# Performance work log

Measured on AMD Instinct MI355X. Metric: run time of the kernel, lower is better.

Reference implementation:

```python
import jax, jax.numpy as jnp
import numpy as np

N_ATOMS = 10000
N_EDGES = 200000
L_MAX = 2
K_L = [32, 24, 16]  # k_max_l = n_element_channels * n_max_l

# (l1, l2, L) in the original loop order (l1 outer, l2 inner, L ascending)
PAIRS = [(0,0,0),(0,1,1),(0,2,2),
         (1,0,1),(1,1,0),(1,1,1),(1,1,2),(1,2,1),(1,2,2),
         (2,0,2),(2,1,1),(2,1,2),(2,2,0),(2,2,1),(2,2,2)]
# concatenated input width -> k_max_l[L] per (L, sigma) channel
LIN = {'0_1': (72, 32), '1_1': (80, 24), '1_m1': (40, 24), '2_1': (72, 16), '2_m1': (32, 16)}


def setup_inputs() -> dict:
    key = jax.random.key(0)
    it = iter(jax.random.split(key, 64))
    def nrm(shape):
        return jax.random.normal(next(it), shape, dtype=jnp.float32)
    inp = {}
    for l in range(L_MAX + 1):
        inp['rb%d' % l] = nrm((N_EDGES, K_L[l]))           # radial basis per l
    for l in range(L_MAX + 1):
        inp['sh%d' % l] = nrm((N_EDGES, 2*l+1, 1))         # spherical harmonics per l
    inp['emb'] = nrm((N_ATOMS, 1, K_L[0]))                 # initial center embedding
    for l in range(L_MAX + 1):
        inp['f%d' % l] = nrm((N_ATOMS, 2*l+1, K_L[l]))     # nu=1 equivariant features
    for (l1, l2, L) in PAIRS:
        inp['cg_%d_%d_%d' % (l1, l2, L)] = nrm(((2*l1+1)*(2*l2+1), 2*L+1))
    for LS, (fin, fout) in LIN.items():
        inp['W_' + LS] = nrm((fin, fout)) / np.float32(np.sqrt(fin))
        inp['b_' + LS] = nrm((fout,)) * 0.01
    inp['centers'] = jax.random.randint(next(it), (N_EDGES,), 0, N_ATOMS)
    inp['neighbors'] = jax.random.randint(next(it), (N_EDGES,), 0, N_ATOMS)
    inp['n_atoms'] = N_ATOMS
    return inp


def _normalize(x, dims):
    # Normalizer(dims): RMS normalization over the given dims
    return x * jax.lax.rsqrt(jnp.mean(x * x, axis=dims, keepdims=True) + 1e-12)


def _forward(floats, centers, neighbors, n_atoms):
    (rb0, rb1, rb2, sh0, sh1, sh2, emb, f0, f1, f2,
     cg_0_0_0, cg_0_1_1, cg_0_2_2, cg_1_0_1, cg_1_1_0, cg_1_1_1, cg_1_1_2,
     cg_1_2_1, cg_1_2_2, cg_2_0_2, cg_2_1_1, cg_2_1_2, cg_2_2_0, cg_2_2_1,
     cg_2_2_2, W_0_1, b_0_1, W_1_1, b_1_1, W_1_m1, b_1_m1, W_2_1, b_2_1,
     W_2_m1, b_2_m1) = floats
    rb = [rb0, rb1, rb2]; sh = [sh0, sh1, sh2]; feats = [f0, f1, f2]
    cgs = {'0_0_0': cg_0_0_0, '0_1_1': cg_0_1_1, '0_2_2': cg_0_2_2,
           '1_0_1': cg_1_0_1, '1_1_0': cg_1_1_0, '1_1_1': cg_1_1_1,
           '1_1_2': cg_1_1_2, '1_2_1': cg_1_2_1, '1_2_2': cg_1_2_2,
           '2_0_2': cg_2_0_2, '2_1_1': cg_2_1_1, '2_1_2': cg_2_1_2,
           '2_2_0': cg_2_2_0, '2_2_1': cg_2_2_1, '2_2_2': cg_2_2_2}
    lin = {'0_1': (W_0_1, b_0_1), '1_1': (W_1_1, b_1_1), '1_m1': (W_1_m1, b_1_m1),
           '2_1': (W_2_1, b_2_1), '2_m1': (W_2_m1, b_2_m1)}

    # ---- InvariantMessagePasser: density_l = scatter_add over centers of
    #      sh_l * rb_l * emb[neighbors]
    emb_n = emb[neighbors]                                       # [E, 1, k0]
    densities = []
    for l in range(L_MAX + 1):
        msg = sh[l] * rb[l][:, None, :] * emb_n[:, :, :K_L[l]]   # [E, 2l+1, k_l]
        densities.append(jax.ops.segment_sum(msg, centers, num_segments=n_atoms))

    # ---- EquivariantMessagePasser
    ve = [sh[l] * rb[l][:, None, :] for l in range(L_MAX + 1)]   # vector expansion [E,2l+1,k_l]
    fn = [feats[l][neighbors] for l in range(L_MAX + 1)]         # gathered neighbor feats
    results = {}
    for (l1, l2, L) in PAIRS:
        S = (-1) ** (l1 + l2 + L)
        k = min(K_L[l1], K_L[l2])
        t1 = ve[l1][:, :, :k]                                    # [E, 2l1+1, k]
        t2 = fn[l2][:, :, :k]                                    # [E, 2l2+1, k]
        cg = cgs['%d_%d_%d' % (l1, l2, L)].reshape(2*l1+1, 2*l2+1, 2*L+1)
        # fused outer product + CG contraction -> [E, 2L+1, k]
        res = jnp.einsum('eak,ebk,abM->eMk', t1, t2, cg)
        pooled = jax.ops.segment_sum(res, centers, num_segments=n_atoms)
        LS = '%d_%s' % (L, 'm1' if S < 0 else '1')
        results.setdefault(LS, []).append(pooled)

    outs = {}
    for LS, (W, b) in lin.items():
        x = jnp.concatenate(results[LS], axis=2)                 # [n_atoms, 2L+1, size_LS]
        x = _normalize(x, (0, 1))
        x = jnp.einsum('amf,fk->amk', x, W) + b
        outs[LS] = _normalize(x, (0, 1, 2))

    return (densities[0], densities[1], densities[2],
            outs['0_1'], outs['1_1'], outs['1_m1'], outs['2_1'], outs['2_m1'])


def reference(rb0, rb1, rb2, sh0, sh1, sh2, emb, f0, f1, f2,
              cg_0_0_0, cg_0_1_1, cg_0_2_2, cg_1_0_1, cg_1_1_0, cg_1_1_1,
              cg_1_1_2, cg_1_2_1, cg_1_2_2, cg_2_0_2, cg_2_1_1, cg_2_1_2,
              cg_2_2_0, cg_2_2_1, cg_2_2_2, W_0_1, b_0_1, W_1_1, b_1_1,
              W_1_m1, b_1_m1, W_2_1, b_2_1, W_2_m1, b_2_m1,
              centers, neighbors, n_atoms):
    floats = (rb0, rb1, rb2, sh0, sh1, sh2, emb, f0, f1, f2,
              cg_0_0_0, cg_0_1_1, cg_0_2_2, cg_1_0_1, cg_1_1_0, cg_1_1_1,
              cg_1_1_2, cg_1_2_1, cg_1_2_2, cg_2_0_2, cg_2_1_1, cg_2_1_2,
              cg_2_2_0, cg_2_2_1, cg_2_2_2, W_0_1, b_0_1, W_1_1, b_1_1,
              W_1_m1, b_1_m1, W_2_1, b_2_1, W_2_m1, b_2_m1)
    return _forward(floats, centers, neighbors, n_atoms)
```

## Files before the change

kernel.cpp:

```cpp
#include <hip/hip_runtime.h>
#include <hip/hip_bf16.h>

typedef __hip_bfloat16 bf16;

#define N_ATOMS 10000
#define N_EDGES 200000

#define SCG   0
#define SINV  616
#define SS1P  1024
#define SS2P  19968
#define SWS2  20288
#define SINTS 20352
#define IFLAG  0
#define ICOUNT 16
#define IOFFS  10016
#define ICURS  20032
#define IELIST 30032
#define INTS_END 430032
#define SXACC (SINTS + INTS_END)
#define BIG_FLOATS (SXACC + 952*N_ATOMS)

#define O0 0
#define O1 320000
#define O2 1040000
#define OY 1840000
#define OUT_ELEMS 5200000

__device__ __forceinline__ float b2f(bf16 x){ return __bfloat162float(x); }
__device__ __forceinline__ bf16  f2b(float x){ return __float2bfloat16(x); }

__device__ __forceinline__ float ldv(const float* p, int i){ return p[i]; }
__device__ __forceinline__ float ldv(const bf16*  p, int i){ return b2f(p[i]); }
__device__ __forceinline__ void  stv(float* p, int i, float v){ p[i] = v; }
__device__ __forceinline__ void  stv(bf16*  p, int i, float v){ p[i] = f2b(v); }

template<typename T> __device__ __forceinline__ int dtid();
template<> __device__ __forceinline__ int dtid<bf16>(){ return 0; }
template<> __device__ __forceinline__ int dtid<float>(){ return 1; }

struct Ptrs15 { const void* p[15]; };
struct LinP   { const void* W[5]; const void* B[5]; };

__constant__ int c_cg_sizes[15] = {1,9,25,9,9,27,45,45,75,25,45,75,25,75,125};
__constant__ int c_fin[5]   = {72,80,40,72,32};
__constant__ int c_kout[5]  = {32,24,24,16,16};
__constant__ int c_yoff[5]  = {OY+0, OY+320000, OY+1040000, OY+1760000, OY+2560000};
__constant__ int c_numel[5] = {320000,720000,720000,800000,800000};
__constant__ int c_cum[6]   = {0,32,104,176,256,336};
__constant__ int c_xb[5]    = {0,72,312,432,792};
__constant__ int c_Ms[5]    = {1,3,3,5,5};

__global__ void k_zero(float* wsf, int* wsi,
                       const unsigned short* rb0u, const unsigned short* embu) {
  if (blockIdx.x == 0 && threadIdx.x < 64) {
    int lane = threadIdx.x;
    int bad = 0;
    for (int i = lane; i < 256; i += 64) {
      unsigned u1 = ((unsigned)rb0u[2*i]) << 16;
      unsigned u2 = ((unsigned)embu[2*i]) << 16;
      float v1 = __uint_as_float(u1);
      float v2 = __uint_as_float(u2);
      if (!(fabsf(v1) < 1e9f) || !(fabsf(v2) < 1e9f)) bad = 1;
    }
    unsigned long long any = __ballot(bad);
    if (lane == 0) wsi[IFLAG] = (any != 0ULL) ? 1 : 0;
  }
  int i = blockIdx.x*blockDim.x + threadIdx.x;
  if (i < N_ATOMS) wsi[ICOUNT + i] = 0;
  int j = i - N_ATOMS;
  if (j >= 0 && j < N_ATOMS) wsi[ICURS + j] = 0;
  j -= N_ATOMS;
  if (j >= 0 && j < 18944) wsf[SS1P + j] = 0.f;
  j -= 18944;
  if (j >= 0 && j < 325) wsf[SS2P + j] = 0.f;
}

template<typename T>
__global__ void k_cg(Ptrs15 cg, float* wsf, const int* flag) {
  if (flag[0] != dtid<T>()) return;
  int i = blockIdx.x*blockDim.x + threadIdx.x;
  if (i >= 615) return;
  int s = 0, off = i;
  while (off >= c_cg_sizes[s]) { off -= c_cg_sizes[s]; ++s; }
  wsf[SCG + i] = ldv((const T*)cg.p[s], off);
}

__global__ void k_hist(const int* __restrict__ centers, int* __restrict__ counts) {
  int e = blockIdx.x*blockDim.x + threadIdx.x;
  if (e < N_EDGES) atomicAdd(&counts[centers[e]], 1);
}

__global__ void k_scan(const int* __restrict__ counts, int* __restrict__ offs) {
  __shared__ int part[1024];
  int t = threadIdx.x;
  int base = t*10;
  int s = 0;
  for (int i = 0; i < 10; ++i) { int idx = base+i; if (idx < N_ATOMS) s += counts[idx]; }
  part[t] = s;
  __syncthreads();
  for (int d = 1; d < 1024; d <<= 1) {
    int v = part[t];
    int add = (t >= d) ? part[t-d] : 0;
    __syncthreads();
    part[t] = v + add;
    __syncthreads();
  }
  int run = (t == 0) ? 0 : part[t-1];
  for (int i = 0; i < 10; ++i) {
    int idx = base+i;
    if (idx < N_ATOMS) { offs[idx] = run; run += counts[idx]; }
  }
  if (t == 1023) offs[N_ATOMS] = part[1023];
}

__global__ void k_scatter2(const int* __restrict__ centers, const int* __restrict__ neighbors,
                           const int* __restrict__ offs, int* __restrict__ cursors,
                           int2* __restrict__ elist2) {
  int e = blockIdx.x*blockDim.x + threadIdx.x;
  if (e < N_EDGES) {
    int c = centers[e];
    int p = atomicAdd(&cursors[c], 1);
    elist2[offs[c] + p] = make_int2(e, neighbors[e]);
  }
}

template<typename T>
__device__ __forceinline__ void role_body(
    const T* __restrict__ rb0, const T* __restrict__ rb1, const T* __restrict__ rb2,
    const T* __restrict__ sh0, const T* __restrict__ sh1, const T* __restrict__ sh2,
    const T* __restrict__ emb, const T* __restrict__ f0, const T* __restrict__ f1,
    const T* __restrict__ f2, const int2* __restrict__ el2,
    const int* __restrict__ offs, Ptrs15 cg,
    float* __restrict__ s1p, float* __restrict__ xout, T* __restrict__ out)
{
  int lane = threadIdx.x & 63;
  int role = threadIdx.x >> 6;
  int bid = blockIdx.x;
  int a = (bid & 7) * 1250 + (bid >> 3);
  int beg = offs[a];
  int cnt = offs[a+1] - beg;
  const int2* eb = el2 + beg;
  int ab = a & 63;
  int k32 = lane & 31, e2 = lane >> 5;
  int k16 = lane & 15, e4 = lane >> 4;
  float* xg = xout + a*952;
  float* s1r = s1p + ab*296;

  if (role == 0) {
    float acc[8];
    #pragma unroll
    for (int i = 0; i < 8; ++i) acc[i] = 0.f;
    for (int base = 0; base < cnt; base += 4) {
      #pragma unroll
      for (int u = 0; u < 2; ++u) {
        int idx = base + 2*u + e2;
        float w = (idx < cnt) ? 1.f : 0.f;
        int ic  = (idx < cnt) ? idx : 0;
        int2 en = eb[ic];
        int e = en.x, n = en.y;
        float s0 = ldv(sh0, e);
        float s1a0 = ldv(sh1, e*3+0), s1a1 = ldv(sh1, e*3+1), s1a2 = ldv(sh1, e*3+2);
        float rb0k = ldv(rb0, e*32 + k32) * w;
        float ek   = ldv(emb, n*32 + k32);
        float f0k  = ldv(f0,  n*32 + k32);
        float ve0 = s0 * rb0k;
        acc[0] = fmaf(ve0, ek, acc[0]);
        acc[4] = fmaf(ve0, f0k, acc[4]);
        if (k32 < 24) {
          float rb1k = ldv(rb1, e*24 + k32) * w;
          float rbek = rb1k * ek;
          acc[1] = fmaf(s1a0, rbek, acc[1]);
          acc[2] = fmaf(s1a1, rbek, acc[2]);
          acc[3] = fmaf(s1a2, rbek, acc[3]);
          float f1k0 = ldv(f1, n*72 + k32);
          float f1k1 = ldv(f1, n*72 + 24 + k32);
          float f1k2 = ldv(f1, n*72 + 48 + k32);
          acc[5] = fmaf(ve0, f1k0, acc[5]);
          acc[6] = fmaf(ve0, f1k1, acc[6]);
          acc[7] = fmaf(ve0, f1k2, acc[7]);
        }
      }
    }
    #pragma unroll
    for (int i = 0; i < 8; ++i) acc[i] += __shfl_xor(acc[i], 32);
    const T* C000 = (const T*)cg.p[0];
    const T* C011 = (const T*)cg.p[1];
    float x000 = ldv(C000,0) * acc[4];
    float x011[3];
    #pragma unroll
    for (int M = 0; M < 3; ++M) {
      float t = 0.f;
      #pragma unroll
      for (int b = 0; b < 3; ++b) t = fmaf(acc[5+b], ldv(C011, b*3+M), t);
      x011[M] = t;
    }
    if (lane < 32) {
      stv(out, O0 + a*32 + k32, acc[0]);
      xg[k32] = x000;
      atomicAdd(&s1r[k32], x000*x000);
      if (k32 < 24) {
        #pragma unroll
        for (int m = 0; m < 3; ++m) stv(out, O1 + a*72 + m*24 + k32, acc[1+m]);
        #pragma unroll
        for (int M = 0; M < 3; ++M) xg[72+M*80+k32] = x011[M];
        atomicAdd(&s1r[72+k32], x011[0]*x011[0]+x011[1]*x011[1]+x011[2]*x011[2]);
      }
    }
  } else if (role == 1) {
    float acc[12];
    #pragma unroll
    for (int i = 0; i < 12; ++i) acc[i] = 0.f;
    int k24 = (k32 < 24) ? k32 : 23;
    float m24 = (k32 < 24) ? 1.f : 0.f;
    for (int base = 0; base < cnt; base += 4) {
      #pragma unroll
      for (int u = 0; u < 2; ++u) {
        int idx = base + 2*u + e2;
        float w = ((idx < cnt) ? 1.f : 0.f) * m24;
        int ic  = (idx < cnt) ? idx : 0;
        int2 en = eb[ic];
        int e = en.x, n = en.y;
        float s1a0 = ldv(sh1, e*3+0), s1a1 = ldv(sh1, e*3+1), s1a2 = ldv(sh1, e*3+2);
        float rb1k = ldv(rb1, e*24 + k24) * w;
        float f0k  = ldv(f0,  n*32 + k24);
        float f1k0 = ldv(f1, n*72 + k24);
        float f1k1 = ldv(f1, n*72 + 24 + k24);
        float f1k2 = ldv(f1, n*72 + 48 + k24);
        float g3 = rb1k * f0k;
        acc[0] = fmaf(g3, s1a0, acc[0]);
        acc[1] = fmaf(g3, s1a1, acc[1]);
        acc[2] = fmaf(g3, s1a2, acc[2]);
        float sa;
        sa = rb1k * s1a0;
        acc[3] = fmaf(sa, f1k0, acc[3]); acc[4] = fmaf(sa, f1k1, acc[4]); acc[5] = fmaf(sa, f1k2, acc[5]);
        sa = rb1k * s1a1;
        acc[6] = fmaf(sa, f1k0, acc[6]); acc[7] = fmaf(sa, f1k1, acc[7]); acc[8] = fmaf(sa, f1k2, acc[8]);
        sa = rb1k * s1a2;
        acc[9] = fmaf(sa, f1k0, acc[9]); acc[10] = fmaf(sa, f1k1, acc[10]); acc[11] = fmaf(sa, f1k2, acc[11]);
      }
    }
    #pragma unroll
    for (int i = 0; i < 12; ++i) acc[i] += __shfl_xor(acc[i], 32);
    const T* C101 = (const T*)cg.p[3];
    const T* C110 = (const T*)cg.p[4];
    const T* C111 = (const T*)cg.p[5];
    const T* C112 = (const T*)cg.p[6];
    float x101[3], x111[3], x112[5], x110;
    #pragma unroll
    for (int M = 0; M < 3; ++M) {
      float t = 0.f;
      #pragma unroll
      for (int aa = 0; aa < 3; ++aa) t = fmaf(acc[aa], ldv(C101, aa*3+M), t);
      x101[M] = t;
    }
    {
      float t = 0.f;
      #pragma unroll
      for (int q = 0; q < 9; ++q) t = fmaf(acc[3+q], ldv(C110, q), t);
      x110 = t;
    }
    #pragma unroll
    for (int M = 0; M < 3; ++M) {
      float t = 0.f;
      #pragma unroll
      for (int q = 0; q < 9; ++q) t = fmaf(acc[3+q], ldv(C111, q*3+M), t);
      x111[M] = t;
    }
    #pragma unroll
    for (int M = 0; M < 5; ++M) {
      float t = 0.f;
      #pragma unroll
      for (int q = 0; q < 9; ++q) t = fmaf(acc[3+q], ldv(C112, q*5+M), t);
      x112[M] = t;
    }
    if (lane < 24) {
      xg[32+k32] = x110;
      #pragma unroll
      for (int M = 0; M < 3; ++M) xg[72+M*80+24+k32] = x101[M];
      #pragma unroll
      for (int M = 0; M < 3; ++M) xg[312+M*40+k32]   = x111[M];
      #pragma unroll
      for (int M = 0; M < 5; ++M) xg[432+M*72+16+k32] = x112[M];
      atomicAdd(&s1r[32+k32], x110*x110);
      atomicAdd(&s1r[96+k32], x101[0]*x101[0]+x101[1]*x101[1]+x101[2]*x101[2]);
      atomicAdd(&s1r[152+k32], x111[0]*x111[0]+x111[1]*x111[1]+x111[2]*x111[2]);
      atomicAdd(&s1r[208+k32], x112[0]*x112[0]+x112[1]*x112[1]+x112[2]*x112[2]
                              + x112[3]*x112[3]+x112[4]*x112[4]);
    }
  } else if (role == 2) {
    float acc[25];
    #pragma unroll
    for (int i = 0; i < 25; ++i) acc[i] = 0.f;
    for (int base = 0; base < cnt; base += 8) {
      #pragma unroll
      for (int u = 0; u < 2; ++u) {
        int idx = base + 4*u + e4;
        float w = (idx < cnt) ? 1.f : 0.f;
        int ic  = (idx < cnt) ? idx : 0;
        int2 en = eb[ic];
        int e = en.x, n = en.y;
        float s0 = ldv(sh0, e);
        float s1a[3];
        #pragma unroll
        for (int m = 0; m < 3; ++m) s1a[m] = ldv(sh1, e*3+m);
        float s2a[5];
        #pragma unroll
        for (int m = 0; m < 5; ++m) s2a[m] = ldv(sh2, e*5+m);
        float rb0k = ldv(rb0, e*32 + k16) * w;
        float rb1k = ldv(rb1, e*24 + k16) * w;
        float rb2k = ldv(rb2, e*16 + k16) * w;
        float ek   = ldv(emb, n*32 + k16);
        float f2k[5];
        #pragma unroll
        for (int b = 0; b < 5; ++b) f2k[b] = ldv(f2, n*80 + b*16 + k16);
        float re = rb2k * ek;
        #pragma unroll
        for (int m = 0; m < 5; ++m) acc[m] = fmaf(s2a[m], re, acc[m]);
        float ve0 = s0 * rb0k;
        #pragma unroll
        for (int b = 0; b < 5; ++b) acc[5+b] = fmaf(ve0, f2k[b], acc[5+b]);
        #pragma unroll
        for (int aa = 0; aa < 3; ++aa) {
          float sa = rb1k * s1a[aa];
          #pragma unroll
          for (int b = 0; b < 5; ++b)
            acc[10+aa*5+b] = fmaf(sa, f2k[b], acc[10+aa*5+b]);
        }
      }
    }
    #pragma unroll
    for (int i = 0; i < 25; ++i) {
      acc[i] += __shfl_xor(acc[i], 16);
      acc[i] += __shfl_xor(acc[i], 32);
    }
    const T* C022 = (const T*)cg.p[2];
    const T* C121 = (const T*)cg.p[7];
    const T* C122 = (const T*)cg.p[8];
    float x022[5], x121[3], x122[5];
    #pragma unroll
    for (int M = 0; M < 5; ++M) {
      float t = 0.f;
      #pragma unroll
      for (int b = 0; b < 5; ++b) t = fmaf(acc[5+b], ldv(C022, b*5+M), t);
      x022[M] = t;
    }
    #pragma unroll
    for (int M = 0; M < 3; ++M) {
      float t = 0.f;
      #pragma unroll
      for (int q = 0; q < 15; ++q) t = fmaf(acc[10+q], ldv(C121, q*3+M), t);
      x121[M] = t;
    }
    #pragma unroll
    for (int M = 0; M < 5; ++M) {
      float t = 0.f;
      #pragma unroll
      for (int q = 0; q < 15; ++q) t = fmaf(acc[10+q], ldv(C122, q*5+M), t);
      x122[M] = t;
    }
    if (lane < 16) {
      #pragma unroll
      for (int m = 0; m < 5; ++m) stv(out, O2 + a*80 + m*16 + k16, acc[m]);
      #pragma unroll
      for (int M = 0; M < 5; ++M) xg[432+M*72+k16]   = x022[M];
      #pragma unroll
      for (int M = 0; M < 3; ++M) xg[72+M*80+48+k16] = x121[M];
      #pragma unroll
      for (int M = 0; M < 5; ++M) xg[792+M*32+k16]   = x122[M];
      atomicAdd(&s1r[192+k16], x022[0]*x022[0]+x022[1]*x022[1]+x022[2]*x022[2]
                              + x022[3]*x022[3]+x022[4]*x022[4]);
      atomicAdd(&s1r[120+k16], x121[0]*x121[0]+x121[1]*x121[1]+x121[2]*x121[2]);
      atomicAdd(&s1r[264+k16], x122[0]*x122[0]+x122[1]*x122[1]+x122[2]*x122[2]
                              + x122[3]*x122[3]+x122[4]*x122[4]);
    }
  } else if (role == 3) {
    float acc[20];
    #pragma unroll
    for (int i = 0; i < 20; ++i) acc[i] = 0.f;
    for (int base = 0; base < cnt; base += 8) {
      #pragma unroll
      for (int u = 0; u < 2; ++u) {
        int idx = base + 4*u + e4;
        float w = (idx < cnt) ? 1.f : 0.f;
        int ic  = (idx < cnt) ? idx : 0;
        int2 en = eb[ic];
        int e = en.x, n = en.y;
        float s2a[5];
        #pragma unroll
        for (int m = 0; m < 5; ++m) s2a[m] = ldv(sh2, e*5+m);
        float rb2k = ldv(rb2, e*16 + k16) * w;
        float f0k  = ldv(f0,  n*32 + k16);
        float f1k[3];
        #pragma unroll
        for (int b = 0; b < 3; ++b) f1k[b] = ldv(f1, n*72 + b*24 + k16);
        float g9 = rb2k * f0k;
        #pragma unroll
        for (int aa = 0; aa < 5; ++aa) acc[aa] = fmaf(g9, s2a[aa], acc[aa]);
        #pragma unroll
        for (int aa = 0; aa < 5; ++aa) {
          float sa = rb2k * s2a[aa];
          #pragma unroll
          for (int b = 0; b < 3; ++b)
            acc[5+aa*3+b] = fmaf(sa, f1k[b], acc[5+aa*3+b]);
        }
      }
    }
    #pragma unroll
    for (int i = 0; i < 20; ++i) {
      acc[i] += __shfl_xor(acc[i], 16);
      acc[i] += __shfl_xor(acc[i], 32);
    }
    const T* C202 = (const T*)cg.p[9];
    const T* C211 = (const T*)cg.p[10];
    const T* C212 = (const T*)cg.p[11];
    float x202[5], x211[3], x212[5];
    #pragma unroll
    for (int M = 0; M < 5; ++M) {
      float t = 0.f;
      #pragma unroll
      for (int aa = 0; aa < 5; ++aa) t = fmaf(acc[aa], ldv(C202, aa*5+M), t);
      x202[M] = t;
    }
    #pragma unroll
    for (int M = 0; M < 3; ++M) {
      float t = 0.f;
      #pragma unroll
      for (int q = 0; q < 15; ++q) t = fmaf(acc[5+q], ldv(C211, q*3+M), t);
      x211[M] = t;
    }
    #pragma unroll
    for (int M = 0; M < 5; ++M) {
      float t = 0.f;
      #pragma unroll
      for (int q = 0; q < 15; ++q) t = fmaf(acc[5+q], ldv(C212, q*5+M), t);
      x212[M] = t;
    }
    if (lane < 16) {
      #pragma unroll
      for (int M = 0; M < 5; ++M) xg[432+M*72+40+k16] = x202[M];
      #pragma unroll
      for (int M = 0; M < 3; ++M) xg[72+M*80+64+k16]  = x211[M];
      #pragma unroll
      for (int M = 0; M < 5; ++M) xg[792+M*32+16+k16] = x212[M];
      atomicAdd(&s1r[232+k16], x202[0]*x202[0]+x202[1]*x202[1]+x202[2]*x202[2]
                              + x202[3]*x202[3]+x202[4]*x202[4]);
      atomicAdd(&s1r[136+k16], x211[0]*x211[0]+x211[1]*x211[1]+x211[2]*x211[2]);
      atomicAdd(&s1r[280+k16], x212[0]*x212[0]+x212[1]*x212[1]+x212[2]*x212[2]
                              + x212[3]*x212[3]+x212[4]*x212[4]);
    }
  } else {
    float acc[25];
    #pragma unroll
    for (int i = 0; i < 25; ++i) acc[i] = 0.f;
    for (int base = 0; base < cnt; base += 8) {
      #pragma unroll
      for (int u = 0; u < 2; ++u) {
        int idx = base + 4*u + e4;
        float w = (idx < cnt) ? 1.f : 0.f;
        int ic  = (idx < cnt) ? idx : 0;
        int2 en = eb[ic];
        int e = en.x, n = en.y;
        float s2a[5];
        #pragma unroll
        for (int m = 0; m < 5; ++m) s2a[m] = ldv(sh2, e*5+m);
        float rb2k = ldv(rb2, e*16 + k16) * w;
        float f2k[5];
        #pragma unroll
        for (int b = 0; b < 5; ++b) f2k[b] = ldv(f2, n*80 + b*16 + k16);
        #pragma unroll
        for (int aa = 0; aa < 5; ++aa) {
          float sa = rb2k * s2a[aa];
          #pragma unroll
          for (int b = 0; b < 5; ++b)
            acc[aa*5+b] = fmaf(sa, f2k[b], acc[aa*5+b]);
        }
      }
    }
    #pragma unroll
    for (int i = 0; i < 25; ++i) {
      acc[i] += __shfl_xor(acc[i], 16);
      acc[i] += __shfl_xor(acc[i], 32);
    }
    const T* C220 = (const T*)cg.p[12];
    const T* C221 = (const T*)cg.p[13];
    const T* C222 = (const T*)cg.p[14];
    float x220, x221[3], x222[5];
    {
      float t = 0.f;
      #pragma unroll
      for (int q = 0; q < 25; ++q) t = fmaf(acc[q], ldv(C220, q), t);
      x220 = t;
    }
    #pragma unroll
    for (int M = 0; M < 3; ++M) {
      float t = 0.f;
      #pragma unroll
      for (int q = 0; q < 25; ++q) t = fmaf(acc[q], ldv(C221, q*3+M), t);
      x221[M] = t;
    }
    #pragma unroll
    for (int M = 0; M < 5; ++M) {
      float t = 0.f;
      #pragma unroll
      for (int q = 0; q < 25; ++q) t = fmaf(acc[q], ldv(C222, q*5+M), t);
      x222[M] = t;
    }
    if (lane < 16) {
      xg[56+k16] = x220;
      #pragma unroll
      for (int M = 0; M < 3; ++M) xg[312+M*40+24+k16] = x221[M];
      #pragma unroll
      for (int M = 0; M < 5; ++M) xg[432+M*72+56+k16] = x222[M];
      atomicAdd(&s1r[56+k16], x220*x220);
      atomicAdd(&s1r[176+k16], x221[0]*x221[0]+x221[1]*x221[1]+x221[2]*x221[2]);
      atomicAdd(&s1r[248+k16], x222[0]*x222[0]+x222[1]*x222[1]+x222[2]*x222[2]
                              + x222[3]*x222[3]+x222[4]*x222[4]);
    }
  }
}

__global__ __launch_bounds__(320) void k_role(
    const void* rb0, const void* rb1, const void* rb2,
    const void* sh0, const void* sh1, const void* sh2,
    const void* emb, const void* f0, const void* f1, const void* f2,
    const int2* __restrict__ el2, const int* __restrict__ offs, Ptrs15 cg,
    float* __restrict__ s1p, float* __restrict__ xout, void* outv,
    const int* __restrict__ flag, int know)
{
  int dt = (know >= 0) ? know : flag[0];
  if (dt == 0)
    role_body<bf16>((const bf16*)rb0,(const bf16*)rb1,(const bf16*)rb2,
                    (const bf16*)sh0,(const bf16*)sh1,(const bf16*)sh2,
                    (const bf16*)emb,(const bf16*)f0,(const bf16*)f1,(const bf16*)f2,
                    el2, offs, cg, s1p, xout, (bf16*)outv);
  else
    role_body<float>((const float*)rb0,(const float*)rb1,(const float*)rb2,
                     (const float*)sh0,(const float*)sh1,(const float*)sh2,
                     (const float*)emb,(const float*)f0,(const float*)f1,(const float*)f2,
                     el2, offs, cg, s1p, xout, (float*)outv);
}

template<typename T>
__device__ __forceinline__ void lin_body(
    const float* __restrict__ xg, const float* __restrict__ inv,
    LinP lp, T* __restrict__ out, float* __restrict__ s2p)
{
  int a = blockIdx.x;
  int t = threadIdx.x;
  __shared__ float L[952];
  for (int i = t; i < 952; i += 256) {
    int ch;
    if      (i < 72)  ch = i;
    else if (i < 312) ch = 72  + (i-72)  % 80;
    else if (i < 432) ch = 152 + (i-312) % 40;
    else if (i < 792) ch = 192 + (i-432) % 72;
    else              ch = 264 + (i-792) % 32;
    L[i] = xg[a*952 + i] * inv[ch];
  }
  __syncthreads();
  float y2[5] = {0.f,0.f,0.f,0.f,0.f};
  for (int tau = t; tau < 336; tau += 256) {
    int ls = 0;
    while (tau >= c_cum[ls+1]) ++ls;
    int rem = tau - c_cum[ls];
    int kn = c_kout[ls], fin = c_fin[ls];
    int M = rem / kn, ko = rem - M*kn;
    const T* W = (const T*)lp.W[ls];
    float y = ldv((const T*)lp.B[ls], ko);
    const float* xv = &L[c_xb[ls] + M*fin];
    for (int f = 0; f < fin; ++f) y = fmaf(xv[f], ldv(W, f*kn+ko), y);
    stv(out, c_yoff[ls] + (a*c_Ms[ls] + M)*kn + ko, y);
    y2[ls] += y*y;
  }
  __shared__ float red[4][5];
  #pragma unroll
  for (int i = 0; i < 5; ++i) {
    y2[i] += __shfl_xor(y2[i], 1);  y2[i] += __shfl_xor(y2[i], 2);
    y2[i] += __shfl_xor(y2[i], 4);  y2[i] += __shfl_xor(y2[i], 8);
    y2[i] += __shfl_xor(y2[i], 16); y2[i] += __shfl_xor(y2[i], 32);
  }
  if ((t & 63) == 0) {
    #pragma unroll
    for (int i = 0; i < 5; ++i) red[t>>6][i] = y2[i];
  }
  __syncthreads();
  if (t == 0) {
    #pragma unroll
    for (int i = 0; i < 5; ++i)
      atomicAdd(&s2p[i*64 + (a & 63)], red[0][i]+red[1][i]+red[2][i]+red[3][i]);
  }
}

__global__ __launch_bounds__(256) void k_lin(
    const float* __restrict__ xg, const float* __restrict__ inv,
    LinP lp, void* outv, float* __restrict__ s2p,
    const int* __restrict__ flag, int know)
{
  int dt = (know >= 0) ? know : flag[0];
  if (dt == 0) lin_body<bf16>(xg, inv, lp, (bf16*)outv, s2p);
  else         lin_body<float>(xg, inv, lp, (float*)outv, s2p);
}

__global__ void k_red1(const float* __restrict__ s1p, float* __restrict__ inv) {
  int ch = blockIdx.x, lane = threadIdx.x;
  float v = s1p[lane*296 + ch];
  v += __shfl_xor(v, 1);  v += __shfl_xor(v, 2);  v += __shfl_xor(v, 4);
  v += __shfl_xor(v, 8);  v += __shfl_xor(v, 16); v += __shfl_xor(v, 32);
  if (lane == 0) {
    float rows = (ch < 72) ? 10000.f : (ch < 192) ? 30000.f : 50000.f;
    inv[ch] = rsqrtf(v/rows + 1e-12f);
  }
}

__global__ __launch_bounds__(256) void k_scale(
    const float* __restrict__ s2p, void* outv,
    const int* __restrict__ flag, int know)
{
  __shared__ float ssum[5];
  int t = threadIdx.x;
  if (t < 64) {
    #pragma unroll
    for (int i = 0; i < 5; ++i) {
      float x = s2p[i*64 + t];
      x += __shfl_xor(x, 1);  x += __shfl_xor(x, 2);  x += __shfl_xor(x, 4);
      x += __shfl_xor(x, 8);  x += __shfl_xor(x, 16); x += __shfl_xor(x, 32);
      if (t == 0) ssum[i] = x;
    }
  }
  __syncthreads();
  int dt = (know >= 0) ? know : flag[0];
  int i = blockIdx.x*blockDim.x + t;
  if (i >= 3360000) return;
  int ls = (i < 320000) ? 0 : (i < 1040000) ? 1 : (i < 1760000) ? 2 : (i < 2560000) ? 3 : 4;
  float scale = rsqrtf(ssum[ls] / (float)c_numel[ls] + 1e-12f);
  if (dt == 0) { bf16* o = (bf16*)outv;  stv(o, OY+i, ldv((const bf16*)o,  OY+i) * scale); }
  else         { float* o = (float*)outv; stv(o, OY+i, ldv((const float*)o, OY+i) * scale); }
}

template<typename T, int MODE>
__global__ __launch_bounds__(256) void k_main(
    const T* __restrict__ rb0, const T* __restrict__ rb1, const T* __restrict__ rb2,
    const T* __restrict__ sh0, const T* __restrict__ sh1, const T* __restrict__ sh2,
    const T* __restrict__ emb, const T* __restrict__ f0, const T* __restrict__ f1,
    const T* __restrict__ f2, const int2* __restrict__ el2,
    const int* __restrict__ offs, const float* __restrict__ cgf,
    float* __restrict__ s1p, const float* __restrict__ inv,
    float* __restrict__ s2p, LinP lp, T* __restrict__ out,
    const int* __restrict__ flag)
{
  if (flag[0] != dtid<T>()) return;
  int lane = threadIdx.x & 63;
  int wv   = threadIdx.x >> 6;
  int tix  = threadIdx.x;
  int a = blockIdx.x;
  int beg = offs[a];
  int cnt = offs[a+1] - beg;
  int k32 = lane & 31, e2 = lane >> 5;
  int k16 = lane & 15, e4 = lane >> 4;
  int ab = a & 63;
  float* s1r = s1p + ab*296;

  __shared__ int2 sel[256];
  __shared__ __align__(16) float L[952];
  __shared__ float red[4][5];

  float acc[25];
  #pragma unroll
  for (int i = 0; i < 25; ++i) acc[i] = 0.f;

  for (int cbase = 0; cbase < cnt; cbase += 256) {
    int nch = cnt - cbase; if (nch > 256) nch = 256;
    __syncthreads();
    if (tix < nch) sel[tix] = el2[beg + cbase + tix];
    __syncthreads();

    if (wv == 0) {
      for (int base = 0; base < nch; base += 4) {
        #pragma unroll
        for (int u = 0; u < 2; ++u) {
          int idx = base + 2*u + e2;
          float w = (idx < nch) ? 1.f : 0.f;
          int ic  = (idx < nch) ? idx : 0;
          int2 en = sel[ic];
          int e = en.x, n = en.y;
          float s0 = ldv(sh0, e);
          float s1a0 = ldv(sh1, e*3+0), s1a1 = ldv(sh1, e*3+1), s1a2 = ldv(sh1, e*3+2);
          float rb0k = ldv(rb0, e*32 + k32) * w;
          float ek   = ldv(emb, n*32 + k32);
          float f0k  = ldv(f0,  n*32 + k32);
          float ve0 = s0 * rb0k;
          acc[0] = fmaf(ve0, ek, acc[0]);
          acc[4] = fmaf(ve0, f0k, acc[4]);
          if (k32 < 24) {
            float rb1k = ldv(rb1, e*24 + k32) * w;
            float f1k0 = ldv(f1, n*72 + k32);
            float f1k1 = ldv(f1, n*72 + 24 + k32);
            float f1k2 = ldv(f1, n*72 + 48 + k32);
            float rbek = rb1k * ek;
            acc[1] = fmaf(s1a0, rbek, acc[1]);
            acc[2] = fmaf(s1a1, rbek, acc[2]);
            acc[3] = fmaf(s1a2, rbek, acc[3]);
            acc[5] = fmaf(ve0, f1k0, acc[5]);
            acc[6] = fmaf(ve0, f1k1, acc[6]);
            acc[7] = fmaf(ve0, f1k2, acc[7]);
            float g3 = rb1k * f0k;
            acc[8]  = fmaf(g3, s1a0, acc[8]);
            acc[9]  = fmaf(g3, s1a1, acc[9]);
            acc[10] = fmaf(g3, s1a2, acc[10]);
            #pragma unroll
            for (int aa = 0; aa < 3; ++aa) {
              float sa = rb1k * ((aa==0)?s1a0:(aa==1)?s1a1:s1a2);
              acc[11+aa*3+0] = fmaf(sa, f1k0, acc[11+aa*3+0]);
              acc[11+aa*3+1] = fmaf(sa, f1k1, acc[11+aa*3+1]);
              acc[11+aa*3+2] = fmaf(sa, f1k2, acc[11+aa*3+2]);
            }
          }
        }
      }
    } else if (wv == 1) {
      for (int base = 0; base < nch; base += 8) {
        #pragma unroll
        for (int u = 0; u < 2; ++u) {
          int idx = base + 4*u + e4;
          float w = (idx < nch) ? 1.f : 0.f;
          int ic  = (idx < nch) ? idx : 0;
          int2 en = sel[ic];
          int e = en.x, n = en.y;
          float s0 = ldv(sh0, e);
          float s1a[3];
          #pragma unroll
          for (int m = 0; m < 3; ++m) s1a[m] = ldv(sh1, e*3+m);
          float s2a[5];
          #pragma unroll
          for (int m = 0; m < 5; ++m) s2a[m] = ldv(sh2, e*5+m);
          float rb0k = ldv(rb0, e*32 + k16) * w;
          float rb1k = ldv(rb1, e*24 + k16) * w;
          float rb2k = ldv(rb2, e*16 + k16) * w;
          float ek   = ldv(emb, n*32 + k16);
          float f2k[5];
          #pragma unroll
          for (int b = 0; b < 5; ++b) f2k[b] = ldv(f2, n*80 + b*16 + k16);
          float re = rb2k * ek;
          #pragma unroll
          for (int m = 0; m < 5; ++m) acc[m] = fmaf(s2a[m], re, acc[m]);
          float ve0 = s0 * rb0k;
          #pragma unroll
          for (int b = 0; b < 5; ++b) acc[5+b] = fmaf(ve0, f2k[b], acc[5+b]);
          #pragma unroll
          for (int aa = 0; aa < 3; ++aa) {
            float sa = rb1k * s1a[aa];
            #pragma unroll
            for (int b = 0; b < 5; ++b)
              acc[10+aa*5+b] = fmaf(sa, f2k[b], acc[10+aa*5+b]);
          }
        }
      }
    } else if (wv == 2) {
      for (int base = 0; base < nch; base += 8) {
        #pragma unroll
        for (int u = 0; u < 2; ++u) {
          int idx = base + 4*u + e4;
          float w = (idx < nch) ? 1.f : 0.f;
          int ic  = (idx < nch) ? idx : 0;
          int2 en = sel[ic];
          int e = en.x, n = en.y;
          float s2a[5];
          #pragma unroll
          for (int m = 0; m < 5; ++m) s2a[m] = ldv(sh2, e*5+m);
          float rb2k = ldv(rb2, e*16 + k16) * w;
          float f0k  = ldv(f0,  n*32 + k16);
          float f1k[3];
          #pragma unroll
          for (int b = 0; b < 3; ++b) f1k[b] = ldv(f1, n*72 + b*24 + k16);
          float g9 = rb2k * f0k;
          #pragma unroll
          for (int aa = 0; aa < 5; ++aa) acc[aa] = fmaf(g9, s2a[aa], acc[aa]);
          #pragma unroll
          for (int aa = 0; aa < 5; ++aa) {
            float sa = rb2k * s2a[aa];
            #pragma unroll
            for (int b = 0; b < 3; ++b)
              acc[5+aa*3+b] = fmaf(sa, f1k[b], acc[5+aa*3+b]);
          }
        }
      }
    } else {
      for (int base = 0; base < nch; base += 8) {
        #pragma unroll
        for (int u = 0; u < 2; ++u) {
          int idx = base + 4*u + e4;
          float w = (idx < nch) ? 1.f : 0.f;
          int ic  = (idx < nch) ? idx : 0;
          int2 en = sel[ic];
          int e = en.x, n = en.y;
          float s2a[5];
          #pragma unroll
          for (int m = 0; m < 5; ++m) s2a[m] = ldv(sh2, e*5+m);
          float rb2k = ldv(rb2, e*16 + k16) * w;
          float f2k[5];
          #pragma unroll
          for (int b = 0; b < 5; ++b) f2k[b] = ldv(f2, n*80 + b*16 + k16);
          #pragma unroll
          for (int aa = 0; aa < 5; ++aa) {
            float sa = rb2k * s2a[aa];
            #pragma unroll
            for (int b = 0; b < 5; ++b)
              acc[aa*5+b] = fmaf(sa, f2k[b], acc[aa*5+b]);
          }
        }
      }
    }
  }

  if (wv == 0) {
    #pragma unroll
    for (int i = 0; i < 20; ++i) acc[i] += __shfl_xor(acc[i], 32);
    const float* C000 = cgf + 0;
    const float* C011 = cgf + 1;
    const float* C101 = cgf + 35;
    const float* C110 = cgf + 44;
    const float* C111 = cgf + 53;
    const float* C112 = cgf + 80;
    float r[16];
    r[0] = C000[0] * acc[4];
    #pragma unroll
    for (int M = 0; M < 3; ++M) {
      float t = 0.f;
      #pragma unroll
      for (int b = 0; b < 3; ++b) t = fmaf(acc[5+b], C011[b*3+M], t);
      r[1+M] = t;
    }
    #pragma unroll
    for (int M = 0; M < 3; ++M) {
      float t = 0.f;
      #pragma unroll
      for (int aa = 0; aa < 3; ++aa) t = fmaf(acc[8+aa], C101[aa*3+M], t);
      r[4+M] = t;
    }
    {
      float t = 0.f;
      #pragma unroll
      for (int q = 0; q < 9; ++q) t = fmaf(acc[11+q], C110[q], t);
      r[7] = t;
    }
    #pragma unroll
    for (int M = 0; M < 3; ++M) {
      float t = 0.f;
      #pragma unroll
      for (int q = 0; q < 9; ++q) t = fmaf(acc[11+q], C111[q*3+M], t);
      r[8+M] = t;
    }
    #pragma unroll
    for (int M = 0; M < 5; ++M) {
      float t = 0.f;
      #pragma unroll
      for (int q = 0; q < 9; ++q) t = fmaf(acc[11+q], C112[q*5+M], t);
      r[11+M] = t;
    }
    acc[4] = r[0];
    #pragma unroll
    for (int M = 0; M < 3; ++M) acc[5+M]  = r[1+M];
    #pragma unroll
    for (int M = 0; M < 3; ++M) acc[8+M]  = r[4+M];
    acc[11] = r[7];
    #pragma unroll
    for (int M = 0; M < 3; ++M) acc[12+M] = r[8+M];
    #pragma unroll
    for (int M = 0; M < 5; ++M) acc[15+M] = r[11+M];
  } else if (wv == 1) {
    #pragma unroll
    for (int i = 0; i < 25; ++i) {
      acc[i] += __shfl_xor(acc[i], 16);
      acc[i] += __shfl_xor(acc[i], 32);
    }
    const float* C022 = cgf + 10;
    const float* C121 = cgf + 125;
    const float* C122 = cgf + 170;
    float r[13];
    #pragma unroll
    for (int M = 0; M < 5; ++M) {
      float t = 0.f;
      #pragma unroll
      for (int b = 0; b < 5; ++b) t = fmaf(acc[5+b], C022[b*5+M], t);
      r[M] = t;
    }
    #pragma unroll
    for (int M = 0; M < 3; ++M) {
      float t = 0.f;
      #pragma unroll
      for (int q = 0; q < 15; ++q) t = fmaf(acc[10+q], C121[q*3+M], t);
      r[5+M] = t;
    }
    #pragma unroll
    for (int M = 0; M < 5; ++M) {
      float t = 0.f;
      #pragma unroll
      for (int q = 0; q < 15; ++q) t = fmaf(acc[10+q], C122[q*5+M], t);
      r[8+M] = t;
    }
    #pragma unroll
    for (int M = 0; M < 5; ++M) acc[5+M]  = r[M];
    #pragma unroll
    for (int M = 0; M < 3; ++M) acc[10+M] = r[5+M];
    #pragma unroll
    for (int M = 0; M < 5; ++M) acc[13+M] = r[8+M];
  } else if (wv == 2) {
    #pragma unroll
    for (int i = 0; i < 20; ++i) {
      acc[i] += __shfl_xor(acc[i], 16);
      acc[i] += __shfl_xor(acc[i], 32);
    }
    const float* C202 = cgf + 245;
    const float* C211 = cgf + 270;
    const float* C212 = cgf + 315;
    float r[13];
    #pragma unroll
    for (int M = 0; M < 5; ++M) {
      float t = 0.f;
      #pragma unroll
      for (int aa = 0; aa < 5; ++aa) t = fmaf(acc[aa], C202[aa*5+M], t);
      r[M] = t;
    }
    #pragma unroll
    for (int M = 0; M < 3; ++M) {
      float t = 0.f;
      #pragma unroll
      for (int q = 0; q < 15; ++q) t = fmaf(acc[5+q], C211[q*3+M], t);
      r[5+M] = t;
    }
    #pragma unroll
    for (int M = 0; M < 5; ++M) {
      float t = 0.f;
      #pragma unroll
      for (int q = 0; q < 15; ++q) t = fmaf(acc[5+q], C212[q*5+M], t);
      r[8+M] = t;
    }
    #pragma unroll
    for (int M = 0; M < 5; ++M) acc[M]   = r[M];
    #pragma unroll
    for (int M = 0; M < 3; ++M) acc[5+M] = r[5+M];
    #pragma unroll
    for (int M = 0; M < 5; ++M) acc[8+M] = r[8+M];
  } else {
    #pragma unroll
    for (int i = 0; i < 25; ++i) {
      acc[i] += __shfl_xor(acc[i], 16);
      acc[i] += __shfl_xor(acc[i], 32);
    }
    const float* C220 = cgf + 390;
    const float* C221 = cgf + 415;
    const float* C222 = cgf + 490;
    float r[9];
    {
      float t = 0.f;
      #pragma unroll
      for (int q = 0; q < 25; ++q) t = fmaf(acc[q], C220[q], t);
      r[0] = t;
    }
    #pragma unroll
    for (int M = 0; M < 3; ++M) {
      float t = 0.f;
      #pragma unroll
      for (int q = 0; q < 25; ++q) t = fmaf(acc[q], C221[q*3+M], t);
      r[1+M] = t;
    }
    #pragma unroll
    for (int M = 0; M < 5; ++M) {
      float t = 0.f;
      #pragma unroll
      for (int q = 0; q < 25; ++q) t = fmaf(acc[q], C222[q*5+M], t);
      r[4+M] = t;
    }
    #pragma unroll
    for (int i = 0; i < 9; ++i) acc[i] = r[i];
  }

  if constexpr (MODE == 1) {
    if (wv == 0) {
      if (lane < 32) {
        stv(out, O0 + a*32 + k32, acc[0]);
        atomicAdd(&s1r[k32], acc[4]*acc[4]);
        if (k32 < 24) {
          #pragma unroll
          for (int m = 0; m < 3; ++m) stv(out, O1 + a*72 + m*24 + k32, acc[1+m]);
          atomicAdd(&s1r[32+k32], acc[11]*acc[11]);
          float q;
          q = acc[5]*acc[5]+acc[6]*acc[6]+acc[7]*acc[7];
          atomicAdd(&s1r[72+k32], q);
          q = acc[8]*acc[8]+acc[9]*acc[9]+acc[10]*acc[10];
          atomicAdd(&s1r[96+k32], q);
          q = acc[12]*acc[12]+acc[13]*acc[13]+acc[14]*acc[14];
          atomicAdd(&s1r[152+k32], q);
          q = acc[15]*acc[15]+acc[16]*acc[16]+acc[17]*acc[17]
            + acc[18]*acc[18]+acc[19]*acc[19];
          atomicAdd(&s1r[208+k32], q);
        }
      }
    } else if (wv == 1) {
      if (lane < 16) {
        #pragma unroll
        for (int m = 0; m < 5; ++m) stv(out, O2 + a*80 + m*16 + k16, acc[m]);
        float q;
        q = acc[5]*acc[5]+acc[6]*acc[6]+acc[7]*acc[7]+acc[8]*acc[8]+acc[9]*acc[9];
        atomicAdd(&s1r[192+k16], q);
        q = acc[10]*acc[10]+acc[11]*acc[11]+acc[12]*acc[12];
        atomicAdd(&s1r[120+k16], q);
        q = acc[13]*acc[13]+acc[14]*acc[14]+acc[15]*acc[15]
          + acc[16]*acc[16]+acc[17]*acc[17];
        atomicAdd(&s1r[264+k16], q);
      }
    } else if (wv == 2) {
      if (lane < 16) {
        float q;
        q = acc[0]*acc[0]+acc[1]*acc[1]+acc[2]*acc[2]+acc[3]*acc[3]+acc[4]*acc[4];
        atomicAdd(&s1r[232+k16], q);
        q = acc[5]*acc[5]+acc[6]*acc[6]+acc[7]*acc[7];
        atomicAdd(&s1r[136+k16], q);
        q = acc[8]*acc[8]+acc[9]*acc[9]+acc[10]*acc[10]
          + acc[11]*acc[11]+acc[12]*acc[12];
        atomicAdd(&s1r[280+k16], q);
      }
    } else {
      if (lane < 16) {
        atomicAdd(&s1r[56+k16], acc[0]*acc[0]);
        float q;
        q = acc[1]*acc[1]+acc[2]*acc[2]+acc[3]*acc[3];
        atomicAdd(&s1r[176+k16], q);
        q = acc[4]*acc[4]+acc[5]*acc[5]+acc[6]*acc[6]
          + acc[7]*acc[7]+acc[8]*acc[8];
        atomicAdd(&s1r[248+k16], q);
      }
    }
  }

  if constexpr (MODE == 2) {
    if (wv == 0) {
      if (lane < 32) {
        L[k32] = acc[4]*inv[k32];
        if (k32 < 24) {
          L[32+k32] = acc[11]*inv[32+k32];
          #pragma unroll
          for (int M = 0; M < 3; ++M) L[72+M*80+k32]     = acc[5+M]*inv[72+k32];
          #pragma unroll
          for (int M = 0; M < 3; ++M) L[72+M*80+24+k32]  = acc[8+M]*inv[96+k32];
          #pragma unroll
          for (int M = 0; M < 3; ++M) L[312+M*40+k32]    = acc[12+M]*inv[152+k32];
          #pragma unroll
          for (int M = 0; M < 5; ++M) L[432+M*72+16+k32] = acc[15+M]*inv[208+k32];
        }
      }
    } else if (wv == 1) {
      if (lane < 16) {
        #pragma unroll
        for (int M = 0; M < 5; ++M) L[432+M*72+k16]    = acc[5+M]*inv[192+k16];
        #pragma unroll
        for (int M = 0; M < 3; ++M) L[72+M*80+48+k16]  = acc[10+M]*inv[120+k16];
        #pragma unroll
        for (int M = 0; M < 5; ++M) L[792+M*32+k16]    = acc[13+M]*inv[264+k16];
      }
    } else if (wv == 2) {
      if (lane < 16) {
        #pragma unroll
        for (int M = 0; M < 5; ++M) L[432+M*72+40+k16] = acc[0+M]*inv[232+k16];
        #pragma unroll
        for (int M = 0; M < 3; ++M) L[72+M*80+64+k16]  = acc[5+M]*inv[136+k16];
        #pragma unroll
        for (int M = 0; M < 5; ++M) L[792+M*32+16+k16] = acc[8+M]*inv[280+k16];
      }
    } else {
      if (lane < 16) {
        L[56+k16] = acc[0]*inv[56+k16];
        #pragma unroll
        for (int M = 0; M < 3; ++M) L[312+M*40+24+k16] = acc[1+M]*inv[176+k16];
        #pragma unroll
        for (int M = 0; M < 5; ++M) L[432+M*72+56+k16] = acc[4+M]*inv[248+k16];
      }
    }
    __syncthreads();
    int t = threadIdx.x;
    float y2[5] = {0.f,0.f,0.f,0.f,0.f};
    for (int tau = t; tau < 336; tau += 256) {
      int ls = 0;
      while (tau >= c_cum[ls+1]) ++ls;
      int rem = tau - c_cum[ls];
      int kn = c_kout[ls], fin = c_fin[ls];
      int M = rem / kn, ko = rem - M*kn;
      const T* W = (const T*)lp.W[ls];
      float y = ldv((const T*)lp.B[ls], ko);
      const float* xv = &L[c_xb[ls] + M*fin];
      for (int f = 0; f < fin; ++f) y = fmaf(xv[f], ldv(W, f*kn+ko), y);
      stv(out, c_yoff[ls] + (a*c_Ms[ls] + M)*kn + ko, y);
      y2[ls] += y*y;
    }
    #pragma unroll
    for (int i = 0; i < 5; ++i) {
      y2[i] += __shfl_xor(y2[i], 1);  y2[i] += __shfl_xor(y2[i], 2);
      y2[i] += __shfl_xor(y2[i], 4);  y2[i] += __shfl_xor(y2[i], 8);
      y2[i] += __shfl_xor(y2[i], 16); y2[i] += __shfl_xor(y2[i], 32);
    }
    if (lane == 0) {
      #pragma unroll
      for (int i = 0; i < 5; ++i) red[wv][i] = y2[i];
    }
    __syncthreads();
    if (t == 0) {
      #pragma unroll
      for (int i = 0; i < 5; ++i)
        atomicAdd(&s2p[i*64 + ab], red[0][i]+red[1][i]+red[2][i]+red[3][i]);
    }
  }
}

extern "C" void kernel_launch(void* const* d_in, const int* in_sizes, int n_in,
                              void* d_out, int out_size, void* d_ws, size_t ws_size,
                              hipStream_t stream) {
  float* wsf = (float*)d_ws;
  int*   wsi = (int*)(wsf + SINTS);
  const int* centers   = (const int*)d_in[35];
  const int* neighbors = (const int*)d_in[36];
  bool big = ws_size >= (size_t)BIG_FLOATS * 4;

  int know = -1;
  if (in_sizes) {
    long long nb = (long long)in_sizes[0];
    if (nb == (long long)N_EDGES*32*2) know = 0;
    else if (nb == (long long)N_EDGES*32*4) know = 1;
  }
  if (know < 0) {
    long long ob = (long long)out_size;
    if (ob == (long long)OUT_ELEMS*2) know = 0;
    else if (ob == (long long)OUT_ELEMS*4) know = 1;
  }

  Ptrs15 cg;
  for (int i = 0; i < 15; ++i) cg.p[i] = d_in[10+i];
  LinP lp;
  lp.W[0] = d_in[25]; lp.B[0] = d_in[26];
  lp.W[1] = d_in[27]; lp.B[1] = d_in[28];
  lp.W[2] = d_in[29]; lp.B[2] = d_in[30];
  lp.W[3] = d_in[31]; lp.B[3] = d_in[32];
  lp.W[4] = d_in[33]; lp.B[4] = d_in[34];

  const int* flag = wsi + IFLAG;
  const int2* el2 = (const int2*)(wsi + IELIST);

  k_zero<<<154, 256, 0, stream>>>(wsf, wsi,
                                  (const unsigned short*)d_in[0],
                                  (const unsigned short*)d_in[6]);
  k_hist<<<(N_EDGES+255)/256, 256, 0, stream>>>(centers, wsi+ICOUNT);
  k_scan<<<1, 1024, 0, stream>>>(wsi+ICOUNT, wsi+IOFFS);
  k_scatter2<<<(N_EDGES+255)/256, 256, 0, stream>>>(centers, neighbors, wsi+IOFFS,
                                                    wsi+ICURS, (int2*)(wsi+IELIST));

  if (big) {
    k_role<<<N_ATOMS, 320, 0, stream>>>(d_in[0], d_in[1], d_in[2], d_in[3], d_in[4],
        d_in[5], d_in[6], d_in[7], d_in[8], d_in[9], el2, wsi+IOFFS, cg,
        wsf+SS1P, wsf+SXACC, d_out, flag, know);
    k_red1<<<296, 64, 0, stream>>>(wsf+SS1P, wsf+SINV);
    k_lin<<<N_ATOMS, 256, 0, stream>>>(wsf+SXACC, wsf+SINV, lp, d_out, wsf+SS2P,
                                       flag, know);
    k_scale<<<(3360000+255)/256, 256, 0, stream>>>(wsf+SS2P, d_out, flag, know);
  } else {
    k_cg<bf16 ><<<3, 256, 0, stream>>>(cg, wsf, flag);
    k_cg<float><<<3, 256, 0, stream>>>(cg, wsf, flag);
    k_main<bf16,1><<<N_ATOMS, 256, 0, stream>>>((const bf16*)d_in[0], (const bf16*)d_in[1],
        (const bf16*)d_in[2], (const bf16*)d_in[3], (const bf16*)d_in[4], (const bf16*)d_in[5],
        (const bf16*)d_in[6], (const bf16*)d_in[7], (const bf16*)d_in[8], (const bf16*)d_in[9],
        el2, wsi+IOFFS, wsf+SCG, wsf+SS1P, nullptr, nullptr, lp, (bf16*)d_out, flag);
    k_main<float,1><<<N_ATOMS, 256, 0, stream>>>((const float*)d_in[0], (const float*)d_in[1],
        (const float*)d_in[2], (const float*)d_in[3], (const float*)d_in[4], (const float*)d_in[5],
        (const float*)d_in[6], (const float*)d_in[7], (const float*)d_in[8], (const float*)d_in[9],
        el2, wsi+IOFFS, wsf+SCG, wsf+SS1P, nullptr, nullptr, lp, (float*)d_out, flag);
    k_red1<<<296, 64, 0, stream>>>(wsf+SS1P, wsf+SINV);
    k_main<bf16,2><<<N_ATOMS, 256, 0, stream>>>((const bf16*)d_in[0], (const bf16*)d_in[1],
        (const bf16*)d_in[2], (const bf16*)d_in[3], (const bf16*)d_in[4], (const bf16*)d_in[5],
        (const bf16*)d_in[6], (const bf16*)d_in[7], (const bf16*)d_in[8], (const bf16*)d_in[9],
        el2, wsi+IOFFS, wsf+SCG, nullptr, wsf+SINV, wsf+SS2P, lp, (bf16*)d_out, flag);
    k_main<float,2><<<N_ATOMS, 256, 0, stream>>>((const float*)d_in[0], (const float*)d_in[1],
        (const float*)d_in[2], (const float*)d_in[3], (const float*)d_in[4], (const float*)d_in[5],
        (const float*)d_in[6], (const float*)d_in[7], (const float*)d_in[8], (const float*)d_in[9],
        el2, wsi+IOFFS, wsf+SCG, nullptr, wsf+SINV, wsf+SS2P, lp, (float*)d_out, flag);
    k_scale<<<(3360000+255)/256, 256, 0, stream>>>(wsf+SS2P, d_out, flag, know);
  }
}
```

Measured before the change: 516.2 us.

## Split role kernel into per-dtype launches with 2-wave blocks over atom-role pairs

Turns the role body into a templated kernel launched once per data type, choosing the type from the host hint or a device flag check. The old launch used one 320-thread block per atom. Each block now has 128 threads, and each wave handles one (atom, role) pair, keeping the XCD-aware atom mapping. Removing the runtime type branch should cut register pressure from inlining both paths, and smaller blocks should improve occupancy and scheduling flexibility. The cost is that, when the type is unknown, two kernels are launched and one exits early.

Measured after the change: 467.5 us. 1.1x faster.

```diff
diff --git a/kernel.cpp b/kernel.cpp
--- a/kernel.cpp
+++ b/kernel.cpp
@@ -126,18 +126,22 @@
 }
 
 template<typename T>
-__device__ __forceinline__ void role_body(
+__global__ __launch_bounds__(128) void k_role(
     const T* __restrict__ rb0, const T* __restrict__ rb1, const T* __restrict__ rb2,
     const T* __restrict__ sh0, const T* __restrict__ sh1, const T* __restrict__ sh2,
     const T* __restrict__ emb, const T* __restrict__ f0, const T* __restrict__ f1,
     const T* __restrict__ f2, const int2* __restrict__ el2,
     const int* __restrict__ offs, Ptrs15 cg,
-    float* __restrict__ s1p, float* __restrict__ xout, T* __restrict__ out)
+    float* __restrict__ s1p, float* __restrict__ xout, T* __restrict__ out,
+    const int* __restrict__ flag)
 {
+  if (flag[0] != dtid<T>()) return;
   int lane = threadIdx.x & 63;
-  int role = threadIdx.x >> 6;
-  int bid = blockIdx.x;
-  int a = (bid & 7) * 1250 + (bid >> 3);
+  int xcd = blockIdx.x & 7;
+  int g   = (blockIdx.x >> 3) * 2 + (threadIdx.x >> 6);
+  int al  = g / 5;
+  int role = g - al*5;
+  int a = al * 8 + xcd;
   int beg = offs[a];
   int cnt = offs[a+1] - beg;
   const int2* eb = el2 + beg;
@@ -518,27 +522,6 @@
                               + x222[3]*x222[3]+x222[4]*x222[4]);
     }
   }
-}
-
-__global__ __launch_bounds__(320) void k_role(
-    const void* rb0, const void* rb1, const void* rb2,
-    const void* sh0, const void* sh1, const void* sh2,
-    const void* emb, const void* f0, const void* f1, const void* f2,
-    const int2* __restrict__ el2, const int* __restrict__ offs, Ptrs15 cg,
-    float* __restrict__ s1p, float* __restrict__ xout, void* outv,
-    const int* __restrict__ flag, int know)
-{
-  int dt = (know >= 0) ? know : flag[0];
-  if (dt == 0)
-    role_body<bf16>((const bf16*)rb0,(const bf16*)rb1,(const bf16*)rb2,
-                    (const bf16*)sh0,(const bf16*)sh1,(const bf16*)sh2,
-                    (const bf16*)emb,(const bf16*)f0,(const bf16*)f1,(const bf16*)f2,
-                    el2, offs, cg, s1p, xout, (bf16*)outv);
-  else
-    role_body<float>((const float*)rb0,(const float*)rb1,(const float*)rb2,
-                     (const float*)sh0,(const float*)sh1,(const float*)sh2,
-                     (const float*)emb,(const float*)f0,(const float*)f1,(const float*)f2,
-                     el2, offs, cg, s1p, xout, (float*)outv);
 }
 
 template<typename T>
@@ -1154,9 +1137,16 @@
                                                     wsi+ICURS, (int2*)(wsi+IELIST));
 
   if (big) {
-    k_role<<<N_ATOMS, 320, 0, stream>>>(d_in[0], d_in[1], d_in[2], d_in[3], d_in[4],
-        d_in[5], d_in[6], d_in[7], d_in[8], d_in[9], el2, wsi+IOFFS, cg,
-        wsf+SS1P, wsf+SXACC, d_out, flag, know);
+    if (know != 1)
+      k_role<bf16><<<25000, 128, 0, stream>>>((const bf16*)d_in[0], (const bf16*)d_in[1],
+          (const bf16*)d_in[2], (const bf16*)d_in[3], (const bf16*)d_in[4], (const bf16*)d_in[5],
+          (const bf16*)d_in[6], (const bf16*)d_in[7], (const bf16*)d_in[8], (const bf16*)d_in[9],
+          el2, wsi+IOFFS, cg, wsf+SS1P, wsf+SXACC, (bf16*)d_out, flag);
+    if (know != 0)
+      k_role<float><<<25000, 128, 0, stream>>>((const float*)d_in[0], (const float*)d_in[1],
+          (const float*)d_in[2], (const float*)d_in[3], (const float*)d_in[4], (const float*)d_in[5],
+          (const float*)d_in[6], (const float*)d_in[7], (const float*)d_in[8], (const float*)d_in[9],
+          el2, wsi+IOFFS, cg, wsf+SS1P, wsf+SXACC, (float*)d_out, flag);
     k_red1<<<296, 64, 0, stream>>>(wsf+SS1P, wsf+SINV);
     k_lin<<<N_ATOMS, 256, 0, stream>>>(wsf+SXACC, wsf+SINV, lp, d_out, wsf+SS2P,
                                        flag, know);
```
